# Kernel optimization log

Hardware: AMD Instinct MI355X
Metric: run time of the kernel (lower is better)

The kernel has to match this reference:

```python
import jax, jax.numpy as jnp
import numpy as np

B, S, T, H, E, V = 32, 400, 32, 512, 128, 50000
A = H  # attention feature dim

def setup_inputs() -> dict:
    key = jax.random.key(0)
    ks = jax.random.split(key, 16)
    f = lambda k, shape: jax.random.normal(k, shape, dtype=jnp.float32) * 0.02
    return {
        "source_tokens": jax.random.randint(ks[0], (B, S), 0, V, dtype=jnp.int32),
        "embedded_tgt": jax.random.normal(ks[1], (B, T, E), dtype=jnp.float32),
        "encoder_states": jax.random.normal(ks[2], (B, S, 2 * H), dtype=jnp.float32),
        "source_mask": jnp.ones((B, S), dtype=bool),
        "h0": f(ks[3], (B, H)),
        "c0": f(ks[4], (B, H)),
        "W_ih": f(ks[5], (4 * H, E)),
        "W_hh": f(ks[6], (4 * H, H)),
        "b_ih": jnp.zeros((4 * H,), jnp.float32),
        "b_hh": jnp.zeros((4 * H,), jnp.float32),
        "W_enc": f(ks[7], (2 * H, A)),
        "W_dec": f(ks[8], (H, A)),
        "w_cov": f(ks[9], (A,)),
        "b_att": jnp.zeros((A,), jnp.float32),
        "v_att": f(ks[10], (A,)),
        "W_ah": f(ks[11], (3 * H, H)),
        "b_ah": jnp.zeros((H,), jnp.float32),
        "W_pg": f(ks[12], (3 * H + E, 1)),
        "b_pg": jnp.zeros((1,), jnp.float32),
        "W_v": f(ks[13], (H, V)),
        "b_v": jnp.zeros((V,), jnp.float32),
    }


def reference(source_tokens, embedded_tgt, encoder_states, source_mask, h0, c0,
              W_ih, W_hh, b_ih, b_hh, W_enc, W_dec, w_cov, b_att, v_att,
              W_ah, b_ah, W_pg, b_pg, W_v, b_v):
    Bn, Sn = source_tokens.shape
    # precompute encoder projection for Bahdanau attention: (B,S,A)
    enc_proj = jnp.einsum('bsd,da->bsa', encoder_states, W_enc)
    bidx = jnp.arange(Bn)[:, None]
    NEG = jnp.float32(-1e9)
    EPS = jnp.float32(1e-20)

    def step(carry, emb):  # emb: (B,E)
        h, c, cov = carry
        # LSTM cell (torch gate order i,f,g,o)
        gates = emb @ W_ih.T + h @ W_hh.T + b_ih + b_hh
        i, fg, g, o = jnp.split(gates, 4, axis=-1)
        c = jax.nn.sigmoid(fg) * c + jax.nn.sigmoid(i) * jnp.tanh(g)
        h = jax.nn.sigmoid(o) * jnp.tanh(c)
        # coverage attention
        feat = jnp.tanh(enc_proj + (h @ W_dec)[:, None, :] + cov[:, :, None] * w_cov + b_att)
        scores = jnp.where(source_mask, feat @ v_att, NEG)  # (B,S)
        attn = jax.nn.softmax(scores, axis=-1)
        context = jnp.einsum('bs,bsd->bd', attn, encoder_states)  # (B,2H)
        cov = cov + attn
        ah = jnp.tanh(jnp.concatenate([context, h], axis=-1) @ W_ah + b_ah)  # (B,H)
        p_gen = jax.nn.sigmoid(jnp.concatenate([context, h, emb], axis=-1) @ W_pg + b_pg)  # (B,1)
        vocab_dist = p_gen * jax.nn.softmax(ah @ W_v + b_v, axis=-1)  # (B,V)
        attn_dist = (1.0 - p_gen) * attn  # (B,S)
        final = vocab_dist.at[bidx, source_tokens].add(attn_dist)  # copy-merge scatter_add
        logp = jnp.log(final + EPS)
        return (h, c, cov), (logp, ah, attn, cov, p_gen[:, 0])

    cov0 = jnp.zeros_like(source_mask, dtype=jnp.float32)
    _, (logps, dec_states, attns, covs, p_gens) = jax.lax.scan(
        step, (h0, c0, cov0), jnp.swapaxes(embedded_tgt, 0, 1))
    tr = lambda x: jnp.swapaxes(x, 0, 1)  # (T,B,...) -> (B,T,...)
    return tr(logps), tr(dec_states), tr(attns), tr(covs), tr(p_gens)
```

## Files before the change

kernel.cpp:

```cpp
#include <hip/hip_runtime.h>
#include <hip/hip_bf16.h>
#include <stdint.h>
#include <stddef.h>

#define B_  32
#define S_  400
#define T_  32
#define H_  512
#define E_  128
#define V_  50000
#define A_  512
#define H2_ 1024
#define H3_ 1536
#define H4_ 2048
#define R_  1024
#define PGK_ 1664
#define NBLKV_ 391
#define GRB_ 128
#define WROW_ 520

typedef unsigned short u16;
typedef short v8s __attribute__((ext_vector_type(8)));
typedef float v4f __attribute__((ext_vector_type(4)));

__device__ __forceinline__ float fsig(float x){ return 1.0f/(1.0f + __expf(-x)); }
__device__ __forceinline__ float ftanh(float x){ float e = __expf(2.0f*x); return 1.0f - 2.0f/(e + 1.0f); }
__device__ __forceinline__ u16 f2bf(float x){ __hip_bfloat16 b = __float2bfloat16(x); return *reinterpret_cast<u16*>(&b); }
__device__ __forceinline__ float bf2f(u16 u){ __hip_bfloat16 b = *reinterpret_cast<__hip_bfloat16*>(&u); return __bfloat162float(b); }

__device__ __forceinline__ float wsum(float v){
  #pragma unroll
  for (int off = 32; off > 0; off >>= 1) v += __shfl_xor(v, off, 64);
  return v;
}
__device__ __forceinline__ float wmax(float v){
  #pragma unroll
  for (int off = 32; off > 0; off >>= 1) v = fmaxf(v, __shfl_xor(v, off, 64));
  return v;
}

#define ALD(p)    __hip_atomic_load((p), __ATOMIC_RELAXED, __HIP_MEMORY_SCOPE_AGENT)
#define AST(p,v)  __hip_atomic_store((p), (v), __ATOMIC_RELAXED, __HIP_MEMORY_SCOPE_AGENT)

__device__ __forceinline__ void ldsbar(){
  asm volatile("s_waitcnt lgkmcnt(0)" ::: "memory");
  __builtin_amdgcn_s_barrier();
  asm volatile("" ::: "memory");
}

__device__ __forceinline__ void gridbar2(unsigned* bar, unsigned target, int grp){
  __syncthreads();
  if (threadIdx.x == 0){
    unsigned v = __hip_atomic_fetch_add(bar + grp*32, 1u, __ATOMIC_RELAXED, __HIP_MEMORY_SCOPE_AGENT);
    if (v == target*16u - 1u){
      unsigned g2 = __hip_atomic_fetch_add(bar + 256, 1u, __ATOMIC_RELAXED, __HIP_MEMORY_SCOPE_AGENT);
      if (g2 == target*8u - 1u)
        AST(bar + 288, target);
    }
    while (ALD(bar + 288) < target) __builtin_amdgcn_s_sleep(2);
    asm volatile("" ::: "memory");
  }
  __syncthreads();
}


__global__ void k_init0(unsigned* __restrict__ bar, unsigned long long* __restrict__ mz){
  int t = threadIdx.x;
  if (t < 512) AST(bar + t, 0u);
  if (t < 128) AST(mz + t, 0ull);
}

__global__ __launch_bounds__(256) void k_transpose(const float* __restrict__ in, float* __restrict__ out, int R, int C){
  __shared__ float tile[64][65];
  int c0 = blockIdx.x*64, r0 = blockIdx.y*64;
  int tid = threadIdx.x;
  int cl = tid & 63, q = tid >> 6;
  #pragma unroll
  for (int i=0;i<16;i++){
    int r = q + i*4;
    float v = 0.0f;
    if (r0 + r < R && c0 + cl < C) v = in[(size_t)(r0+r)*C + c0 + cl];
    tile[r][cl] = v;
  }
  __syncthreads();
  #pragma unroll
  for (int i=0;i<16;i++){
    int c = q + i*4;
    if (c0 + c < C && r0 + cl < R)
      out[(size_t)(c0+c)*R + r0 + cl] = tile[cl][c];
  }
}

__global__ __launch_bounds__(256) void k_convT(const float* __restrict__ in, u16* __restrict__ hi, int R, int C){
  __shared__ float tile[64][65];
  int c0 = blockIdx.x*64, r0 = blockIdx.y*64;
  int tid = threadIdx.x;
  int cl = tid & 63, q = tid >> 6;
  #pragma unroll
  for (int i=0;i<16;i++){
    int r = q + i*4;
    float v = 0.0f;
    if (r0 + r < R && c0 + cl < C) v = in[(size_t)(r0+r)*C + c0 + cl];
    tile[r][cl] = v;
  }
  __syncthreads();
  #pragma unroll
  for (int i=0;i<16;i++){
    int c = q + i*4;
    if (c0 + c < C && r0 + cl < R)
      hi[(size_t)(c0+c)*R + r0 + cl] = f2bf(tile[cl][c]);
  }
}

__global__ __launch_bounds__(256) void k_convT3(const float* __restrict__ in, u16* __restrict__ out){
  __shared__ float tile[64][65];
  int c0 = blockIdx.x*64, r0 = blockIdx.y*64;
  int tid = threadIdx.x;
  int cl = tid & 63, q = tid >> 6;
  #pragma unroll
  for (int i=0;i<16;i++){
    int r = q + i*4;
    tile[r][cl] = in[(size_t)(r0+r)*A_ + c0 + cl];
  }
  __syncthreads();
  #pragma unroll
  for (int i=0;i<16;i++){
    int c = q + i*4;
    float v = tile[cl][c];
    u16 h = f2bf(v);
    u16 lo = f2bf(v - bf2f(h));
    size_t o = (size_t)(c0+c)*3072 + (r0+cl);
    out[o] = h;
    out[o + 1024] = lo;
    out[o + 2048] = h;
  }
}

__global__ void k_conv3(const float* __restrict__ in, u16* __restrict__ out, int n4){
  int i = blockIdx.x*256 + threadIdx.x;
  if (i >= n4) return;
  float4 x = reinterpret_cast<const float4*>(in)[i];
  u16 h0v=f2bf(x.x), h1v=f2bf(x.y), h2v=f2bf(x.z), h3v=f2bf(x.w);
  uint2 hv; hv.x = (unsigned)h0v | ((unsigned)h1v << 16); hv.y = (unsigned)h2v | ((unsigned)h3v << 16);
  uint2 lv;
  lv.x = (unsigned)f2bf(x.x - bf2f(h0v)) | ((unsigned)f2bf(x.y - bf2f(h1v)) << 16);
  lv.y = (unsigned)f2bf(x.z - bf2f(h2v)) | ((unsigned)f2bf(x.w - bf2f(h3v)) << 16);
  int row = i >> 8, c = (i & 255)*4;
  size_t base = (size_t)row*3072 + c;
  *reinterpret_cast<uint2*>(out + base)        = hv;
  *reinterpret_cast<uint2*>(out + base + 1024) = hv;
  *reinterpret_cast<uint2*>(out + base + 2048) = lv;
}

__global__ __launch_bounds__(256) void k_gih(const float* __restrict__ emb, const float* __restrict__ WihT,
    const float* __restrict__ b_ih, const float* __restrict__ b_hh, float* __restrict__ G){
  __shared__ float em[8][128];
  int r0 = blockIdx.x*8;
  int tid = threadIdx.x;
  #pragma unroll
  for (int i=0;i<4;i++){
    int e = i*256 + tid;
    em[e>>7][e&127] = emb[(size_t)(r0 + (e>>7))*E_ + (e&127)];
  }
  __syncthreads();
  for (int jj=0;jj<8;jj++){
    int j = jj*256 + tid;
    float bias = b_ih[j] + b_hh[j];
    float acc[8];
    #pragma unroll
    for (int r=0;r<8;r++) acc[r] = bias;
    for (int e=0;e<128;e++){
      float wv = WihT[(size_t)e*H4_ + j];
      #pragma unroll
      for (int r=0;r<8;r++) acc[r] += em[r][e]*wv;
    }
    #pragma unroll
    for (int rr=0;rr<8;rr++){
      int r = r0 + rr;
      G[(size_t)(r & 31)*65536 + (size_t)(j >> 9)*16384 + (size_t)(j & 511)*32 + (r >> 5)] = acc[rr];
    }
  }
}

__global__ __launch_bounds__(256, 2) void k_gemm_bf16(
    const u16* __restrict__ A, int lda, const u16* __restrict__ Bt, int ldb,
    const float* __restrict__ bias, float* __restrict__ Cf, u16* __restrict__ Cbf, int ldc,
    int M, int N, int K, float2* __restrict__ stats, int nblk)
{
  __shared__ __align__(16) float CsF[128*132];
  __shared__ float rs[128], rs2[128];
  u16* As = reinterpret_cast<u16*>(CsF);
  u16* Bs = As + 128*64;
  const int tid = threadIdx.x;
  const int m0 = blockIdx.y * 128;
  const int n0 = blockIdx.x * 128;
  const int l  = tid & 63;
  const int wavebase = tid & ~63;
  const int wid = tid >> 6;
  const int wm = (wid >> 1) * 64;
  const int wn = (wid & 1) * 64;

  v4f acc[4][4];
  v4f vzero = {0.0f, 0.0f, 0.0f, 0.0f};
  #pragma unroll
  for (int i=0;i<4;i++)
    #pragma unroll
    for (int j=0;j<4;j++) acc[i][j] = vzero;

  for (int k0 = 0; k0 < K; k0 += 64){
    __syncthreads();
    #pragma unroll
    for (int jj=0;jj<4;jj++){
      int fc = jj*256 + tid;
      int row = fc >> 3;
      int cc = (fc & 7) ^ (row & 7);
      const u16* g = A + (size_t)(m0 + row)*lda + k0 + cc*8;
      __builtin_amdgcn_global_load_lds(
        (__attribute__((address_space(1))) void*)g,
        (__attribute__((address_space(3))) void*)(As + (size_t)(jj*256 + wavebase)*8),
        16, 0, 0);
    }
    #pragma unroll
    for (int jj=0;jj<4;jj++){
      int fc = jj*256 + tid;
      int row = fc >> 3;
      int cc = (fc & 7) ^ (row & 7);
      int rn = n0 + row; if (rn > N-1) rn = N-1;
      const u16* g = Bt + (size_t)rn*ldb + k0 + cc*8;
      __builtin_amdgcn_global_load_lds(
        (__attribute__((address_space(1))) void*)g,
        (__attribute__((address_space(3))) void*)(Bs + (size_t)(jj*256 + wavebase)*8),
        16, 0, 0);
    }
    __syncthreads();
    #pragma unroll
    for (int ks=0;ks<2;ks++){
      v8s af[4], bfr[4];
      #pragma unroll
      for (int rt=0;rt<4;rt++){
        int r = wm + rt*16 + (l & 15);
        int cs = (ks*4 + (l >> 4)) ^ (r & 7);
        af[rt] = *reinterpret_cast<const v8s*>(As + r*64 + cs*8);
      }
      #pragma unroll
      for (int nt=0;nt<4;nt++){
        int r = wn + nt*16 + (l & 15);
        int cs = (ks*4 + (l >> 4)) ^ (r & 7);
        bfr[nt] = *reinterpret_cast<const v8s*>(Bs + r*64 + cs*8);
      }
      #pragma unroll
      for (int rt=0;rt<4;rt++)
        #pragma unroll
        for (int nt=0;nt<4;nt++)
          acc[rt][nt] = __builtin_amdgcn_mfma_f32_16x16x32_bf16(af[rt], bfr[nt], acc[rt][nt], 0, 0, 0);
    }
  }

  const int cl = l & 15;
  const int rg = (l >> 4) * 4;
  float cvv[4][4][4];
  #pragma unroll
  for (int rt=0;rt<4;rt++)
    #pragma unroll
    for (int nt=0;nt<4;nt++){
      int gc = n0 + wn + nt*16 + cl;
      float bv = (bias && gc < N) ? bias[gc] : 0.0f;
      #pragma unroll
      for (int i=0;i<4;i++) cvv[rt][nt][i] = acc[rt][nt][i] + bv;
    }

  if (stats){
    float tsm[4][4];
    #pragma unroll
    for (int rt=0;rt<4;rt++)
      #pragma unroll
      for (int i=0;i<4;i++){
        float mx = -1e30f;
        #pragma unroll
        for (int nt=0;nt<4;nt++){
          int gc = n0 + wn + nt*16 + cl;
          if (gc < N) mx = fmaxf(mx, cvv[rt][nt][i]);
        }
        #pragma unroll
        for (int off=1; off<16; off<<=1) mx = fmaxf(mx, __shfl_xor(mx, off, 64));
        if (wn == 0 && cl == 0) rs[wm + rt*16 + rg + i] = mx;
        tsm[rt][i] = mx;
      }
    __syncthreads();
    if (wn != 0){
      #pragma unroll
      for (int rt=0;rt<4;rt++)
        #pragma unroll
        for (int i=0;i<4;i++){
          float c = fmaxf(tsm[rt][i], rs[wm + rt*16 + rg + i]);
          if (cl == 0) rs[wm + rt*16 + rg + i] = c;
        }
    }
    __syncthreads();
    #pragma unroll
    for (int rt=0;rt<4;rt++)
      #pragma unroll
      for (int i=0;i<4;i++){
        float rm = rs[wm + rt*16 + rg + i];
        float sm = 0.0f;
        #pragma unroll
        for (int nt=0;nt<4;nt++){
          int gc = n0 + wn + nt*16 + cl;
          if (gc < N) sm += __expf(cvv[rt][nt][i] - rm);
        }
        #pragma unroll
        for (int off=1; off<16; off<<=1) sm += __shfl_xor(sm, off, 64);
        tsm[rt][i] = sm;
        if (wn == 0 && cl == 0) rs2[wm + rt*16 + rg + i] = sm;
      }
    __syncthreads();
    if (wn != 0 && cl == 0){
      #pragma unroll
      for (int rt=0;rt<4;rt++)
        #pragma unroll
        for (int i=0;i<4;i++){
          int row = wm + rt*16 + rg + i;
          stats[(size_t)(m0 + row)*nblk + blockIdx.x] =
            make_float2(rs[row], tsm[rt][i] + rs2[row]);
        }
    }
  }

  __syncthreads();
  #pragma unroll
  for (int rt=0;rt<4;rt++)
    #pragma unroll
    for (int nt=0;nt<4;nt++)
      #pragma unroll
      for (int i=0;i<4;i++)
        CsF[(wm + rt*16 + rg + i)*132 + wn + nt*16 + cl] = cvv[rt][nt][i];
  __syncthreads();
  #pragma unroll
  for (int it=0; it<16; ++it){
    int row = (tid >> 5) + it*8;
    int c4 = tid & 31;
    int gc = n0 + c4*4;
    int gr = m0 + row;
    if (gc < N){
      float4 v = *reinterpret_cast<const float4*>(&CsF[row*132 + c4*4]);
      if (Cf) *reinterpret_cast<float4*>(Cf + (size_t)gr*ldc + gc) = v;
      if (Cbf){
        uint2 o;
        o.x = (unsigned)f2bf(v.x) | ((unsigned)f2bf(v.y) << 16);
        o.y = (unsigned)f2bf(v.z) | ((unsigned)f2bf(v.w) << 16);
        *reinterpret_cast<uint2*>(Cbf + (size_t)gr*ldc + gc) = o;
      }
    }
  }
}

__global__ __launch_bounds__(256) void k_wv_f32(
  const float* __restrict__ Aah, const float* __restrict__ Wv, const float* __restrict__ bv,
  float* __restrict__ Cl)
{
  __shared__ float Asf[32][68];
  __shared__ float Bsf[32][64];
  int n0 = blockIdx.x*64, m0 = blockIdx.y*64;
  int tid = threadIdx.x;
  int tx = tid & 15, ty = tid >> 4;
  float acc[4][4] = {};
  for (int kc = 0; kc < H_; kc += 32){
    __syncthreads();
    #pragma unroll
    for (int i=0;i<8;i++){
      int e = i*256 + tid;
      Asf[e & 31][e >> 5] = Aah[(size_t)(m0 + (e >> 5))*H_ + kc + (e & 31)];
    }
    #pragma unroll
    for (int i=0;i<8;i++){
      int e = i*256 + tid;
      int nc = n0 + (e & 63); if (nc >= V_) nc = V_-1;
      Bsf[e >> 6][e & 63] = Wv[(size_t)(kc + (e >> 6))*V_ + nc];
    }
    __syncthreads();
    #pragma unroll
    for (int k=0;k<32;k++){
      float4 a4 = *reinterpret_cast<const float4*>(&Asf[k][ty*4]);
      float4 b4 = *reinterpret_cast<const float4*>(&Bsf[k][tx*4]);
      float av[4] = {a4.x, a4.y, a4.z, a4.w};
      float bv4[4] = {b4.x, b4.y, b4.z, b4.w};
      #pragma unroll
      for (int i=0;i<4;i++)
        #pragma unroll
        for (int j=0;j<4;j++)
          acc[i][j] = __builtin_fmaf(av[i], bv4[j], acc[i][j]);
    }
  }
  #pragma unroll
  for (int i=0;i<4;i++){
    int rr = m0 + ty*4 + i;
    #pragma unroll
    for (int j=0;j<4;j++){
      int cc = n0 + tx*4 + j;
      if (cc < V_) Cl[(size_t)rr*V_ + cc] = acc[i][j] + bv[cc];
    }
  }
}

__global__ __launch_bounds__(1024) void k_recur(
  const float* __restrict__ W_hh, const float* __restrict__ G2,
  const float* __restrict__ W_decT, const u16* __restrict__ ep_bf,
  const float* __restrict__ w_cov, const float* __restrict__ v_att,
  const void* __restrict__ maskp, const float* __restrict__ h0,
  const float* __restrict__ c0, float* __restrict__ h_gT,
  float* __restrict__ dec_g, unsigned long long* __restrict__ mz,
  float* __restrict__ catbuf, float* __restrict__ attns, float* __restrict__ covs,
  unsigned* __restrict__ bar)
{
  const int beta = blockIdx.x;
  const int tid = threadIdx.x;
  __shared__ __align__(16) u16 Whi[32*WROW_];
  __shared__ __align__(16) u16 Wlo[32*WROW_];
  __shared__ __align__(16) u16 Hhi[32*WROW_];
  __shared__ __align__(16) u16 Hlo[32*WROW_];
  __shared__ float gv2[16][32];
  __shared__ float c_l[128];
  __shared__ float dec_l[512];
  __shared__ float sc_l[100];
  __shared__ float cov_l[100];
  __shared__ float smz[4][2];

  const int b32 = tid & 31;
  const int w = tid >> 6, l = tid & 63;
  const int grp = beta & 7;
  const int bb = (beta & 7)*4 + (beta >> 5);
  const int sq = (beta >> 3) & 3;
  const int b2 = (tid & 15)*2;
  const int kg = tid >> 4;

  for (int idx = tid; idx < 32*512; idx += 1024){
    int row = idx >> 9;
    int k = idx & 511;
    float v = 0.0f;
    if (row < 16)      v = W_hh[((size_t)(row >> 2)*H_ + beta*4 + (row & 3))*H_ + k];
    else if (row < 20) v = W_decT[(size_t)(beta*4 + (row - 16))*H_ + k];
    u16 h = f2bf(v);
    Whi[row*WROW_ + k] = h;
    Wlo[row*WROW_ + k] = f2bf(v - bf2f(h));
  }
  if (tid < 128) c_l[tid] = c0[(size_t)(tid & 31)*H_ + beta*4 + (tid >> 5)];
  if (tid < 100) cov_l[tid] = 0.f;

  const unsigned* m32p = (const unsigned*)maskp;
  const unsigned char* m8p = (const unsigned char*)maskp;
  const bool bytemode = (m32p[0] == 0x01010101u);

  float wc8[8], va8[8];
  {
    int a0 = l*8;
    #pragma unroll
    for (int j=0;j<8;j++){ wc8[j] = w_cov[a0+j]; va8[j] = v_att[a0+j]; }
  }

  float hA[8], hB[8];
  unsigned long long hld[8];
  #pragma unroll
  for (int kk=0;kk<8;kk++){
    int k = kg*8 + kk;
    hA[kk] = h0[(size_t)b2*H_ + k];
    hB[kk] = h0[(size_t)(b2+1)*H_ + k];
  }

  unsigned gen = 0;
  for (int i = 0; i <= T_; ++i){
    const int par = i & 1;
    {
      v8s phA, plA, phB, plB;
      #pragma unroll
      for (int kk=0;kk<8;kk++){
        float va = hA[kk], vb = hB[kk];
        u16 ha = f2bf(va), hb = f2bf(vb);
        phA[kk] = (short)ha; plA[kk] = (short)f2bf(va - bf2f(ha));
        phB[kk] = (short)hb; plB[kk] = (short)f2bf(vb - bf2f(hb));
      }
      *reinterpret_cast<v8s*>(Hhi + (size_t)b2*WROW_ + kg*8) = phA;
      *reinterpret_cast<v8s*>(Hlo + (size_t)b2*WROW_ + kg*8) = plA;
      *reinterpret_cast<v8s*>(Hhi + (size_t)(b2+1)*WROW_ + kg*8) = phB;
      *reinterpret_cast<v8s*>(Hlo + (size_t)(b2+1)*WROW_ + kg*8) = plB;
    }
    ldsbar();

    if (w < 4){
      const int mt = w >> 1, nt = w & 1;
      const int fr = (l & 15);
      const int fo = (l >> 4)*8;
      const u16* Ahi = Whi + (size_t)(mt*16 + fr)*WROW_ + fo;
      const u16* Alo = Wlo + (size_t)(mt*16 + fr)*WROW_ + fo;
      const u16* Bhi = Hhi + (size_t)(nt*16 + fr)*WROW_ + fo;
      const u16* Blo = Hlo + (size_t)(nt*16 + fr)*WROW_ + fo;
      v4f a0 = {0.f,0.f,0.f,0.f}, a1 = a0, a2 = a0;
      #pragma unroll
      for (int ks=0; ks<16; ks++){
        v8s wh = *reinterpret_cast<const v8s*>(Ahi + ks*32);
        v8s wl = *reinterpret_cast<const v8s*>(Alo + ks*32);
        v8s hh = *reinterpret_cast<const v8s*>(Bhi + ks*32);
        v8s hl = *reinterpret_cast<const v8s*>(Blo + ks*32);
        a0 = __builtin_amdgcn_mfma_f32_16x16x32_bf16(wh, hh, a0, 0, 0, 0);
        a1 = __builtin_amdgcn_mfma_f32_16x16x32_bf16(wh, hl, a1, 0, 0, 0);
        a2 = __builtin_amdgcn_mfma_f32_16x16x32_bf16(wl, hh, a2, 0, 0, 0);
      }
      v4f acc = a0 + a1 + a2;
      if (mt == 0){
        int col = nt*16 + fr;
        int r0w = (l >> 4)*4;
        #pragma unroll
        for (int q=0;q<4;q++) gv2[r0w + q][col] = acc[q];
      } else if ((l >> 4) == 0){
        int b = nt*16 + fr;
        float* dg = dec_g + (size_t)par*B_*A_ + (size_t)b*A_ + beta*4;
        unsigned long long p0 = ((unsigned long long)__float_as_uint(acc[1]) << 32) | __float_as_uint(acc[0]);
        unsigned long long p1 = ((unsigned long long)__float_as_uint(acc[3]) << 32) | __float_as_uint(acc[2]);
        AST(reinterpret_cast<unsigned long long*>(dg), p0);
        AST(reinterpret_cast<unsigned long long*>(dg + 2), p1);
      }
    }
    ldsbar();

    if (i < T_ && tid < 128){
      int hh = tid >> 5;
      int hidx = beta*4 + hh;
      const float* Gr = G2 + (size_t)i*65536 + (size_t)hidx*32 + b32;
      float gi = gv2[0*4+hh][b32] + Gr[0];
      float gf = gv2[1*4+hh][b32] + Gr[16384];
      float gz = gv2[2*4+hh][b32] + Gr[32768];
      float go = gv2[3*4+hh][b32] + Gr[49152];
      float co = c_l[tid];
      float cn = fsig(gf)*co + fsig(gi)*ftanh(gz);
      float hn = fsig(go)*ftanh(cn);
      c_l[tid] = cn;
      AST(h_gT + (size_t)(par^1)*16384 + (size_t)hidx*32 + b32, hn);
      catbuf[(size_t)(b32*T_ + i)*H3_ + H2_ + hidx] = hn;
    }
    gridbar2(bar, ++gen, grp);

    if (i < T_){
      const unsigned long long* hp =
        reinterpret_cast<const unsigned long long*>(h_gT + (size_t)(par^1)*16384);
      #pragma unroll
      for (int kk=0;kk<8;kk++)
        hld[kk] = ALD(hp + (size_t)(kg*8 + kk)*16 + (b2 >> 1));
    }

    if (i > 0){
      const int r = bb*T_ + (i-1);
      if (tid < 512) dec_l[tid] = ALD(dec_g + (size_t)par*B_*A_ + (size_t)bb*A_ + tid);
      ldsbar();
      int a0i = l*8;
      float dec8[8];
      #pragma unroll
      for (int j=0;j<8;j++) dec8[j] = dec_l[a0i+j];
      #pragma unroll
      for (int it=0; it<7; ++it){
        int sl = w + it*16;
        if (sl < 100){
          int s = sq*100 + sl;
          float cv = cov_l[sl];
          uint4 e8 = *reinterpret_cast<const uint4*>(ep_bf + (size_t)(bb*S_ + s)*A_ + a0i);
          unsigned uu[4] = {e8.x, e8.y, e8.z, e8.w};
          float part = 0.f;
          #pragma unroll
          for (int j=0;j<4;j++){
            float xa = bf2f((u16)(uu[j] & 0xFFFFu)) + dec8[2*j]   + cv*wc8[2*j];
            part += va8[2*j]*ftanh(xa);
            float xb = bf2f((u16)(uu[j] >> 16))     + dec8[2*j+1] + cv*wc8[2*j+1];
            part += va8[2*j+1]*ftanh(xb);
          }
          part = wsum(part);
          if (l == 0){
            bool on = bytemode ? (m8p[bb*S_+s] != 0) : (m32p[bb*S_+s] != 0u);
            sc_l[sl] = on ? part : -1e9f;
          }
        }
      }
      __syncthreads();
      if (tid < 64){
        float x1v = sc_l[l];
        float x2v = (l + 64 < 100) ? sc_l[l + 64] : -1e30f;
        float m = wmax(fmaxf(x1v, x2v));
        float z = __expf(x1v - m) + ((l + 64 < 100) ? __expf(x2v - m) : 0.f);
        z = wsum(z);
        if (l == 0){
          unsigned zt = (__float_as_uint(z) & ~255u) | (gen & 255u);
          unsigned long long pk = ((unsigned long long)zt << 32) | (unsigned long long)__float_as_uint(m);
          AST(mz + bb*4 + sq, pk);
        }
      }
      if (tid < 4){
        unsigned long long v;
        do {
          v = ALD(mz + bb*4 + tid);
          if (((unsigned)(v >> 32) & 255u) == (gen & 255u)) break;
          __builtin_amdgcn_s_sleep(1);
        } while (true);
        smz[tid][0] = __uint_as_float((unsigned)v);
        smz[tid][1] = __uint_as_float((unsigned)(v >> 32));
      }
      __syncthreads();
      float gm = fmaxf(fmaxf(smz[0][0], smz[1][0]), fmaxf(smz[2][0], smz[3][0]));
      float gZ = smz[0][1]*__expf(smz[0][0]-gm) + smz[1][1]*__expf(smz[1][0]-gm)
               + smz[2][1]*__expf(smz[2][0]-gm) + smz[3][1]*__expf(smz[3][0]-gm);
      float invZ = 1.f/gZ;
      if (tid < 100){
        float av = __expf(sc_l[tid] - gm)*invZ;
        int s = sq*100 + tid;
        float cn = cov_l[tid] + av;
        cov_l[tid] = cn;
        attns[(size_t)r*S_ + s] = av;
        covs[(size_t)r*S_ + s]  = cn;
      }
      __syncthreads();
    }

    if (i < T_){
      #pragma unroll
      for (int kk=0;kk<8;kk++){
        hA[kk] = __uint_as_float((unsigned)hld[kk]);
        hB[kk] = __uint_as_float((unsigned)(hld[kk] >> 32));
      }
    }
  }
}


__global__ __launch_bounds__(256, 2) void k_ctx(
  const float* __restrict__ attns, const float* __restrict__ enc, float* __restrict__ catbuf)
{
  __shared__ float att_s[32][400];
  int d0 = blockIdx.x*64, b = blockIdx.y;
  int tid = threadIdx.x;
  for (int tt=0; tt<32; ++tt)
    for (int s = tid; s < S_; s += 256)
      att_s[tt][s] = attns[(size_t)(b*T_ + tt)*S_ + s];
  __syncthreads();
  int d = d0 + (tid & 63);
  int t0 = (tid >> 6)*8;
  float acc[8] = {0,0,0,0,0,0,0,0};
  const float* encb = enc + (size_t)b*S_*H2_ + d;
  #pragma unroll 4
  for (int s=0; s<S_; ++s){
    float ev = encb[(size_t)s*H2_];
    #pragma unroll
    for (int i=0;i<8;i++) acc[i] = __builtin_fmaf(att_s[t0+i][s], ev, acc[i]);
  }
  #pragma unroll
  for (int i=0;i<8;i++)
    catbuf[(size_t)(b*T_ + t0 + i)*H3_ + d] = acc[i];
}

__global__ __launch_bounds__(256) void k_ahgemm(
  const float* __restrict__ Acat, const float* __restrict__ W_ah, const float* __restrict__ b_ah,
  float* __restrict__ dec_states, u16* __restrict__ ah_bf)
{
  __shared__ float Asf[32][68];
  __shared__ float Bsf[32][64];
  int n0 = blockIdx.x*64, m0 = blockIdx.y*64;
  int tid = threadIdx.x;
  int tx = tid & 15, ty = tid >> 4;
  float acc[4][4] = {};
  for (int kc = 0; kc < H3_; kc += 32){
    __syncthreads();
    #pragma unroll
    for (int i=0;i<8;i++){
      int e = i*256 + tid;
      Asf[e & 31][e >> 5] = Acat[(size_t)(m0 + (e >> 5))*H3_ + kc + (e & 31)];
    }
    #pragma unroll
    for (int i=0;i<8;i++){
      int e = i*256 + tid;
      Bsf[e >> 6][e & 63] = W_ah[(size_t)(kc + (e >> 6))*H_ + n0 + (e & 63)];
    }
    __syncthreads();
    #pragma unroll
    for (int k=0;k<32;k++){
      float4 a4 = *reinterpret_cast<const float4*>(&Asf[k][ty*4]);
      float4 b4 = *reinterpret_cast<const float4*>(&Bsf[k][tx*4]);
      float av[4] = {a4.x, a4.y, a4.z, a4.w};
      float bv[4] = {b4.x, b4.y, b4.z, b4.w};
      #pragma unroll
      for (int i=0;i<4;i++)
        #pragma unroll
        for (int j=0;j<4;j++)
          acc[i][j] = __builtin_fmaf(av[i], bv[j], acc[i][j]);
    }
  }
  #pragma unroll
  for (int i=0;i<4;i++){
    int rr = m0 + ty*4 + i;
    #pragma unroll
    for (int j=0;j<4;j++){
      int cc = n0 + tx*4 + j;
      float v = ftanh(acc[i][j] + b_ah[cc]);
      dec_states[(size_t)rr*H_ + cc] = v;
      if (ah_bf) ah_bf[(size_t)rr*H_ + cc] = f2bf(v);
    }
  }
}

__global__ __launch_bounds__(512) void k_pgen(const float* __restrict__ catbuf, const float* __restrict__ emb,
  const float* __restrict__ W_pg, const float* __restrict__ b_pg, float* __restrict__ pgens)
{
  int w = threadIdx.x >> 6, l = threadIdx.x & 63;
  int r = blockIdx.x*8 + w;
  float part = 0.0f;
  for (int d = l; d < PGK_; d += 64){
    float x = (d < H3_) ? catbuf[(size_t)r*H3_ + d] : emb[(size_t)r*E_ + (d - H3_)];
    part += x*W_pg[d];
  }
  part = wsum(part);
  if (l == 0) pgens[r] = fsig(part + b_pg[0]);
}

__global__ __launch_bounds__(512) void k_final2(
  float* __restrict__ logits, const float* __restrict__ pgens,
  const float* __restrict__ attns, const int* __restrict__ src,
  const float2* __restrict__ stats, int nblk)
{
  __shared__ unsigned bits[1568];
  __shared__ unsigned keys[1024];
  __shared__ float vals[1024];
  __shared__ float sred[18];
  int r = blockIdx.x;
  int b = r >> 5;
  int tid = threadIdx.x;
  int w = tid >> 6, l = tid & 63;
  float* row = logits + (size_t)r*V_;

  for (int i = tid; i < 1568; i += 512) bits[i] = 0u;
  for (int i = tid; i < 1024; i += 512){ keys[i] = 0xFFFFFFFFu; vals[i] = 0.0f; }

  if (stats){
    float m = -1e30f, Z = 0.0f;
    if (tid < nblk){ float2 st = stats[(size_t)r*nblk + tid]; m = st.x; Z = st.y; }
    #pragma unroll
    for (int off=32; off>0; off>>=1){
      float mo = __shfl_xor(m, off, 64);
      float Zo = __shfl_xor(Z, off, 64);
      float nm = fmaxf(m, mo);
      Z = Z*__expf(m - nm) + Zo*__expf(mo - nm);
      m = nm;
    }
    if (l == 0){ sred[w*2] = m; sred[w*2+1] = Z; }
    __syncthreads();
    if (tid == 0){
      float gm = -1e30f, gz = 0.0f;
      #pragma unroll
      for (int i=0;i<8;i++){
        float mi = sred[i*2], zi = sred[i*2+1];
        float nm = fmaxf(gm, mi);
        gz = gz*__expf(gm - nm) + zi*__expf(mi - nm);
        gm = nm;
      }
      sred[16] = gm; sred[17] = gz;
    }
    __syncthreads();
  } else {
    float m = -1e30f;
    for (int j = tid; j < V_/4; j += 512){
      float4 x = reinterpret_cast<const float4*>(row)[j];
      m = fmaxf(fmaxf(m, x.x), fmaxf(fmaxf(x.y, x.z), x.w));
    }
    m = wmax(m);
    if (l == 0) sred[w] = m;
    __syncthreads();
    if (tid == 0){
      float gm = -1e30f;
      #pragma unroll
      for (int i=0;i<8;i++) gm = fmaxf(gm, sred[i]);
      sred[16] = gm;
    }
    __syncthreads();
    float gm = sred[16];
    float z = 0.0f;
    for (int j = tid; j < V_/4; j += 512){
      float4 x = reinterpret_cast<const float4*>(row)[j];
      z += __expf(x.x-gm) + __expf(x.y-gm) + __expf(x.z-gm) + __expf(x.w-gm);
    }
    z = wsum(z);
    if (l == 0) sred[8 + w] = z;
    __syncthreads();
    if (tid == 0){
      float gz = 0.0f;
      #pragma unroll
      for (int i=0;i<8;i++) gz += sred[8 + i];
      sred[17] = gz;
    }
    __syncthreads();
  }

  float gm = sred[16];
  float gZ = sred[17];
  float pg = pgens[r];
  float scale = pg / gZ;
  float lscale = __logf(scale);

  if (tid < S_){
    int tok = src[b*S_ + tid];
    float add = (1.0f - pg)*attns[(size_t)r*S_ + tid];
    atomicOr(&bits[tok >> 5], 1u << (tok & 31));
    unsigned h = ((unsigned)tok * 2654435761u) >> 22;
    while (true){
      unsigned prev = atomicCAS(&keys[h], 0xFFFFFFFFu, (unsigned)tok);
      if (prev == 0xFFFFFFFFu || prev == (unsigned)tok){
        atomicAdd(&vals[h], add);
        break;
      }
      h = (h + 1) & 1023;
    }
  }
  __syncthreads();

  for (int j = tid; j < V_/4; j += 512){
    float4 x = reinterpret_cast<const float4*>(row)[j];
    int v = 4*j;
    float o[4];
    float xv[4] = {x.x, x.y, x.z, x.w};
    #pragma unroll
    for (int k=0;k<4;k++){
      int vv = v + k;
      bool hit = (bits[vv >> 5] >> (vv & 31)) & 1u;
      float tt = xv[k] - gm + lscale;
      if (!hit && tt > -25.0f){
        o[k] = tt;
      } else {
        float pval = __expf(xv[k] - gm)*scale;
        if (hit){
          unsigned h = ((unsigned)vv * 2654435761u) >> 22;
          while (keys[h] != 0xFFFFFFFFu){
            if (keys[h] == (unsigned)vv){ pval += vals[h]; break; }
            h = (h + 1) & 1023;
          }
        }
        o[k] = __logf(pval + 1e-20f);
      }
    }
    reinterpret_cast<float4*>(row)[j] = make_float4(o[0], o[1], o[2], o[3]);
  }
}


extern "C" void kernel_launch(void* const* d_in, const int* in_sizes, int n_in,
                              void* d_out, int out_size, void* d_ws, size_t ws_size,
                              hipStream_t stream)
{
  const int* src_tokens = (const int*)d_in[0];
  const float* embedded = (const float*)d_in[1];
  const float* enc      = (const float*)d_in[2];
  const void*  maskp    = (const void*)d_in[3];
  const float* h0  = (const float*)d_in[4];
  const float* c0  = (const float*)d_in[5];
  const float* W_ih = (const float*)d_in[6];
  const float* W_hh = (const float*)d_in[7];
  const float* b_ih = (const float*)d_in[8];
  const float* b_hh = (const float*)d_in[9];
  const float* W_enc = (const float*)d_in[10];
  const float* W_dec = (const float*)d_in[11];
  const float* w_cov = (const float*)d_in[12];
  const float* b_att = (const float*)d_in[13];
  const float* v_att = (const float*)d_in[14];
  const float* W_ah  = (const float*)d_in[15];
  const float* b_ah  = (const float*)d_in[16];
  const float* W_pg  = (const float*)d_in[17];
  const float* b_pg  = (const float*)d_in[18];
  const float* W_v   = (const float*)d_in[19];
  const float* b_v   = (const float*)d_in[20];
  (void)in_sizes; (void)n_in; (void)out_size;

  float* outp = (float*)d_out;
  float* logps = outp;
  float* dec_states = logps + (size_t)R_*V_;
  float* attns = dec_states + (size_t)R_*H_;
  float* covs  = attns + (size_t)R_*S_;
  float* pgens = covs + (size_t)R_*S_;

  char* sp = (char*)logps;
  auto salloc = [&](size_t bytes) -> void* {
    void* p = (void*)sp;
    sp += (bytes + 255) & ~(size_t)255;
    return p;
  };
  unsigned* bar = (unsigned*)salloc(2048);
  unsigned long long* mz = (unsigned long long*)salloc((size_t)B_*4*8);
  u16* ep_bf    = (u16*)salloc((size_t)B_*S_*A_*2);
  u16* enc3     = (u16*)salloc((size_t)B_*S_*3072*2);
  u16* WencT3   = (u16*)salloc((size_t)A_*3072*2);
  float* WihT   = (float*)salloc((size_t)E_*H4_*4);
  float* W_decT = (float*)salloc((size_t)H_*A_*4);
  float* G2     = (float*)salloc((size_t)R_*H4_*4);
  float* catbuf = (float*)salloc((size_t)R_*H3_*4);
  float* dec_g  = (float*)salloc((size_t)2*B_*A_*4);
  float* h_gT   = (float*)salloc((size_t)2*H_*B_*4);

  char* wp = (char*)d_ws;
  auto walloc = [&](size_t bytes) -> void* {
    void* p = (void*)wp;
    wp += (bytes + 255) & ~(size_t)255;
    return p;
  };
  u16* ah_bf = (u16*)walloc((size_t)R_*H_*2);
  u16* WvT   = (u16*)walloc((size_t)V_*H_*2);
  float2* stats = (float2*)walloc((size_t)R_*NBLKV_*8);
  const size_t ws_fast  = (size_t)R_*H_*2 + (size_t)V_*H_*2 + 512;
  const size_t ws_stats = ws_fast + (size_t)R_*NBLKV_*8 + 256;
  const bool fast_wv   = (ws_size >= ws_fast);
  const bool use_stats = (ws_size >= ws_stats);

  k_init0<<<1, 512, 0, stream>>>(bar, mz);
  k_transpose<<<dim3(2,32), 256, 0, stream>>>(W_ih, WihT, H4_, E_);
  k_transpose<<<dim3(8,8), 256, 0, stream>>>(W_dec, W_decT, H_, A_);
  k_gih<<<128, 256, 0, stream>>>(embedded, WihT, b_ih, b_hh, G2);
  k_conv3<<<(B_*S_*H2_/4 + 255)/256, 256, 0, stream>>>(enc, enc3, B_*S_*H2_/4);
  k_convT3<<<dim3(8,16), 256, 0, stream>>>(W_enc, WencT3);
  if (fast_wv)
    k_convT<<<dim3((V_+63)/64, 8), 256, 0, stream>>>(W_v, WvT, H_, V_);

  k_gemm_bf16<<<dim3(A_/128, (B_*S_)/128), 256, 0, stream>>>(
      enc3, 3072, WencT3, 3072, b_att, nullptr, ep_bf, A_, B_*S_, A_, 3072, nullptr, 0);

  k_recur<<<GRB_, 1024, 0, stream>>>(W_hh, G2, W_decT, ep_bf, w_cov, v_att, maskp,
                                     h0, c0, h_gT, dec_g, mz,
                                     catbuf, attns, covs, bar);

  k_ctx<<<dim3(16, 32), 256, 0, stream>>>(attns, enc, catbuf);
  k_ahgemm<<<dim3(8,16), 256, 0, stream>>>(catbuf, W_ah, b_ah, dec_states, fast_wv ? ah_bf : (u16*)nullptr);
  k_pgen<<<128, 512, 0, stream>>>(catbuf, embedded, W_pg, b_pg, pgens);

  if (fast_wv)
    k_gemm_bf16<<<dim3(NBLKV_, R_/128), 256, 0, stream>>>(
        ah_bf, H_, WvT, H_, b_v, logps, nullptr, V_, R_, V_, H_,
        use_stats ? stats : nullptr, NBLKV_);
  else
    k_wv_f32<<<dim3((V_+63)/64, R_/64), 256, 0, stream>>>(dec_states, W_v, b_v, logps);

  k_final2<<<R_, 512, 0, stream>>>(logps, pgens, attns, src_tokens,
                                   (fast_wv && use_stats) ? stats : nullptr, NBLKV_);
}
```

Baseline: 1.194 ms.

## Split recurrent kernel into LSTM producer blocks and per-batch attention consumer blocks

The persistent recurrence kernel is split into 128 LSTM blocks and 32 attention blocks, one per batch row. The LSTM blocks advance through timesteps writing per-step h and decoder projections to step-indexed buffers, and only the LSTM blocks arrive at the barrier. Attention blocks poll the barrier one step behind and compute the full 400-position softmax locally, which removes the cross-block max/sum exchange. This takes attention off the LSTM critical path and lets the two run pipelined, at the cost of more grid blocks, per-step history buffers, and each attention block doing 4x more positions serially.

```diff
diff --git a/kernel.cpp b/kernel.cpp
--- a/kernel.cpp
+++ b/kernel.cpp
@@ -16,7 +16,8 @@
 #define R_  1024
 #define PGK_ 1664
 #define NBLKV_ 391
-#define GRB_ 128
+#define GRBX_ 128
+#define GRB_  160
 #define WROW_ 520
 
 typedef unsigned short u16;
@@ -48,8 +49,7 @@
   asm volatile("" ::: "memory");
 }
 
-__device__ __forceinline__ void gridbar2(unsigned* bar, unsigned target, int grp){
-  __syncthreads();
+__device__ __forceinline__ void arrive(unsigned* bar, unsigned target, int grp){
   if (threadIdx.x == 0){
     unsigned v = __hip_atomic_fetch_add(bar + grp*32, 1u, __ATOMIC_RELAXED, __HIP_MEMORY_SCOPE_AGENT);
     if (v == target*16u - 1u){
@@ -57,6 +57,10 @@
       if (g2 == target*8u - 1u)
         AST(bar + 288, target);
     }
+  }
+}
+__device__ __forceinline__ void pollgate(unsigned* bar, unsigned target){
+  if (threadIdx.x == 0){
     while (ALD(bar + 288) < target) __builtin_amdgcn_s_sleep(2);
     asm volatile("" ::: "memory");
   }
@@ -64,10 +68,9 @@
 }
 
 
-__global__ void k_init0(unsigned* __restrict__ bar, unsigned long long* __restrict__ mz){
+__global__ void k_init0(unsigned* __restrict__ bar){
   int t = threadIdx.x;
   if (t < 512) AST(bar + t, 0u);
-  if (t < 128) AST(mz + t, 0ull);
 }
 
 __global__ __launch_bounds__(256) void k_transpose(const float* __restrict__ in, float* __restrict__ out, int R, int C){
@@ -407,8 +410,8 @@
   const float* __restrict__ W_decT, const u16* __restrict__ ep_bf,
   const float* __restrict__ w_cov, const float* __restrict__ v_att,
   const void* __restrict__ maskp, const float* __restrict__ h0,
-  const float* __restrict__ c0, float* __restrict__ h_gT,
-  float* __restrict__ dec_g, unsigned long long* __restrict__ mz,
+  const float* __restrict__ c0, float* __restrict__ h_steps,
+  float* __restrict__ dec_steps,
   float* __restrict__ catbuf, float* __restrict__ attns, float* __restrict__ covs,
   unsigned* __restrict__ bar)
 {
@@ -421,207 +424,202 @@
   __shared__ float gv2[16][32];
   __shared__ float c_l[128];
   __shared__ float dec_l[512];
-  __shared__ float sc_l[100];
-  __shared__ float cov_l[100];
-  __shared__ float smz[4][2];
+  __shared__ float sc_l[400];
+  __shared__ float cov_l[400];
+  __shared__ float red[16];
 
   const int b32 = tid & 31;
   const int w = tid >> 6, l = tid & 63;
-  const int grp = beta & 7;
-  const int bb = (beta & 7)*4 + (beta >> 5);
-  const int sq = (beta >> 3) & 3;
-  const int b2 = (tid & 15)*2;
-  const int kg = tid >> 4;
-
-  for (int idx = tid; idx < 32*512; idx += 1024){
-    int row = idx >> 9;
-    int k = idx & 511;
-    float v = 0.0f;
-    if (row < 16)      v = W_hh[((size_t)(row >> 2)*H_ + beta*4 + (row & 3))*H_ + k];
-    else if (row < 20) v = W_decT[(size_t)(beta*4 + (row - 16))*H_ + k];
-    u16 h = f2bf(v);
-    Whi[row*WROW_ + k] = h;
-    Wlo[row*WROW_ + k] = f2bf(v - bf2f(h));
-  }
-  if (tid < 128) c_l[tid] = c0[(size_t)(tid & 31)*H_ + beta*4 + (tid >> 5)];
-  if (tid < 100) cov_l[tid] = 0.f;
-
-  const unsigned* m32p = (const unsigned*)maskp;
-  const unsigned char* m8p = (const unsigned char*)maskp;
-  const bool bytemode = (m32p[0] == 0x01010101u);
-
-  float wc8[8], va8[8];
-  {
-    int a0 = l*8;
-    #pragma unroll
-    for (int j=0;j<8;j++){ wc8[j] = w_cov[a0+j]; va8[j] = v_att[a0+j]; }
-  }
-
-  float hA[8], hB[8];
-  unsigned long long hld[8];
-  #pragma unroll
-  for (int kk=0;kk<8;kk++){
-    int k = kg*8 + kk;
-    hA[kk] = h0[(size_t)b2*H_ + k];
-    hB[kk] = h0[(size_t)(b2+1)*H_ + k];
-  }
-
-  unsigned gen = 0;
-  for (int i = 0; i <= T_; ++i){
-    const int par = i & 1;
+
+  if (beta < GRBX_){
+    const int grp = beta & 7;
+    const int b2 = (tid & 15)*2;
+    const int kg = tid >> 4;
+
+    for (int idx = tid; idx < 32*512; idx += 1024){
+      int row = idx >> 9;
+      int k = idx & 511;
+      float v = 0.0f;
+      if (row < 16)      v = W_hh[((size_t)(row >> 2)*H_ + beta*4 + (row & 3))*H_ + k];
+      else if (row < 20) v = W_decT[(size_t)(beta*4 + (row - 16))*H_ + k];
+      u16 h = f2bf(v);
+      Whi[row*WROW_ + k] = h;
+      Wlo[row*WROW_ + k] = f2bf(v - bf2f(h));
+    }
+    if (tid < 128) c_l[tid] = c0[(size_t)(tid & 31)*H_ + beta*4 + (tid >> 5)];
+
+    float hA[8], hB[8];
+    #pragma unroll
+    for (int kk=0;kk<8;kk++){
+      int k = kg*8 + kk;
+      hA[kk] = h0[(size_t)b2*H_ + k];
+      hB[kk] = h0[(size_t)(b2+1)*H_ + k];
+    }
+    __syncthreads();
+
+    for (int i = 0; i <= T_; ++i){
+      if (i > 0){
+        pollgate(bar, (unsigned)i);
+        unsigned long long hld[8];
+        const unsigned long long* hp =
+          reinterpret_cast<const unsigned long long*>(h_steps + (size_t)i*16384);
+        #pragma unroll
+        for (int kk=0;kk<8;kk++)
+          hld[kk] = ALD(hp + (size_t)(kg*8 + kk)*16 + (b2 >> 1));
+        #pragma unroll
+        for (int kk=0;kk<8;kk++){
+          hA[kk] = __uint_as_float((unsigned)hld[kk]);
+          hB[kk] = __uint_as_float((unsigned)(hld[kk] >> 32));
+        }
+      }
+      {
+        v8s phA, plA, phB, plB;
+        #pragma unroll
+        for (int kk=0;kk<8;kk++){
+          float va = hA[kk], vb = hB[kk];
+          u16 ha = f2bf(va), hb = f2bf(vb);
+          phA[kk] = (short)ha; plA[kk] = (short)f2bf(va - bf2f(ha));
+          phB[kk] = (short)hb; plB[kk] = (short)f2bf(vb - bf2f(hb));
+        }
+        *reinterpret_cast<v8s*>(Hhi + (size_t)b2*WROW_ + kg*8) = phA;
+        *reinterpret_cast<v8s*>(Hlo + (size_t)b2*WROW_ + kg*8) = plA;
+        *reinterpret_cast<v8s*>(Hhi + (size_t)(b2+1)*WROW_ + kg*8) = phB;
+        *reinterpret_cast<v8s*>(Hlo + (size_t)(b2+1)*WROW_ + kg*8) = plB;
+      }
+      ldsbar();
+
+      if (w < 4){
+        const int mt = w >> 1, nt = w & 1;
+        const int fr = (l & 15);
+        const int fo = (l >> 4)*8;
+        const u16* Ahi = Whi + (size_t)(mt*16 + fr)*WROW_ + fo;
+        const u16* Alo = Wlo + (size_t)(mt*16 + fr)*WROW_ + fo;
+        const u16* Bhi = Hhi + (size_t)(nt*16 + fr)*WROW_ + fo;
+        const u16* Blo = Hlo + (size_t)(nt*16 + fr)*WROW_ + fo;
+        v4f a0 = {0.f,0.f,0.f,0.f}, a1 = a0, a2 = a0;
+        #pragma unroll
+        for (int ks=0; ks<16; ks++){
+          v8s wh = *reinterpret_cast<const v8s*>(Ahi + ks*32);
+          v8s wl = *reinterpret_cast<const v8s*>(Alo + ks*32);
+          v8s hh = *reinterpret_cast<const v8s*>(Bhi + ks*32);
+          v8s hl = *reinterpret_cast<const v8s*>(Blo + ks*32);
+          a0 = __builtin_amdgcn_mfma_f32_16x16x32_bf16(wh, hh, a0, 0, 0, 0);
+          a1 = __builtin_amdgcn_mfma_f32_16x16x32_bf16(wh, hl, a1, 0, 0, 0);
+          a2 = __builtin_amdgcn_mfma_f32_16x16x32_bf16(wl, hh, a2, 0, 0, 0);
+        }
+        v4f acc = a0 + a1 + a2;
+        if (mt == 0){
+          int col = nt*16 + fr;
+          int r0w = (l >> 4)*4;
+          #pragma unroll
+          for (int q=0;q<4;q++) gv2[r0w + q][col] = acc[q];
+        } else if ((l >> 4) == 0 && i > 0){
+          int b = nt*16 + fr;
+          float* dg = dec_steps + (size_t)(i-1)*B_*A_ + (size_t)b*A_ + beta*4;
+          unsigned long long p0 = ((unsigned long long)__float_as_uint(acc[1]) << 32) | __float_as_uint(acc[0]);
+          unsigned long long p1 = ((unsigned long long)__float_as_uint(acc[3]) << 32) | __float_as_uint(acc[2]);
+          AST(reinterpret_cast<unsigned long long*>(dg), p0);
+          AST(reinterpret_cast<unsigned long long*>(dg + 2), p1);
+        }
+      }
+      ldsbar();
+
+      if (i < T_ && tid < 128){
+        int hh = tid >> 5;
+        int hidx = beta*4 + hh;
+        const float* Gr = G2 + (size_t)i*65536 + (size_t)hidx*32 + b32;
+        float gi = gv2[0*4+hh][b32] + Gr[0];
+        float gf = gv2[1*4+hh][b32] + Gr[16384];
+        float gz = gv2[2*4+hh][b32] + Gr[32768];
+        float go = gv2[3*4+hh][b32] + Gr[49152];
+        float co = c_l[tid];
+        float cn = fsig(gf)*co + fsig(gi)*ftanh(gz);
+        float hn = fsig(go)*ftanh(cn);
+        c_l[tid] = cn;
+        AST(h_steps + (size_t)(i+1)*16384 + (size_t)hidx*32 + b32, hn);
+        catbuf[(size_t)(b32*T_ + i)*H3_ + H2_ + hidx] = hn;
+      }
+      __syncthreads();
+      arrive(bar, (unsigned)(i+1), grp);
+    }
+  } else {
+    const int bb = beta - GRBX_;
+    if (tid < 400) cov_l[tid] = 0.f;
+
+    const unsigned* m32p = (const unsigned*)maskp;
+    const unsigned char* m8p = (const unsigned char*)maskp;
+    const bool bytemode = (m32p[0] == 0x01010101u);
+
+    float wc8[8], va8[8];
     {
-      v8s phA, plA, phB, plB;
-      #pragma unroll
-      for (int kk=0;kk<8;kk++){
-        float va = hA[kk], vb = hB[kk];
-        u16 ha = f2bf(va), hb = f2bf(vb);
-        phA[kk] = (short)ha; plA[kk] = (short)f2bf(va - bf2f(ha));
-        phB[kk] = (short)hb; plB[kk] = (short)f2bf(vb - bf2f(hb));
-      }
-      *reinterpret_cast<v8s*>(Hhi + (size_t)b2*WROW_ + kg*8) = phA;
-      *reinterpret_cast<v8s*>(Hlo + (size_t)b2*WROW_ + kg*8) = plA;
-      *reinterpret_cast<v8s*>(Hhi + (size_t)(b2+1)*WROW_ + kg*8) = phB;
-      *reinterpret_cast<v8s*>(Hlo + (size_t)(b2+1)*WROW_ + kg*8) = plB;
-    }
-    ldsbar();
-
-    if (w < 4){
-      const int mt = w >> 1, nt = w & 1;
-      const int fr = (l & 15);
-      const int fo = (l >> 4)*8;
-      const u16* Ahi = Whi + (size_t)(mt*16 + fr)*WROW_ + fo;
-      const u16* Alo = Wlo + (size_t)(mt*16 + fr)*WROW_ + fo;
-      const u16* Bhi = Hhi + (size_t)(nt*16 + fr)*WROW_ + fo;
-      const u16* Blo = Hlo + (size_t)(nt*16 + fr)*WROW_ + fo;
-      v4f a0 = {0.f,0.f,0.f,0.f}, a1 = a0, a2 = a0;
-      #pragma unroll
-      for (int ks=0; ks<16; ks++){
-        v8s wh = *reinterpret_cast<const v8s*>(Ahi + ks*32);
-        v8s wl = *reinterpret_cast<const v8s*>(Alo + ks*32);
-        v8s hh = *reinterpret_cast<const v8s*>(Bhi + ks*32);
-        v8s hl = *reinterpret_cast<const v8s*>(Blo + ks*32);
-        a0 = __builtin_amdgcn_mfma_f32_16x16x32_bf16(wh, hh, a0, 0, 0, 0);
-        a1 = __builtin_amdgcn_mfma_f32_16x16x32_bf16(wh, hl, a1, 0, 0, 0);
-        a2 = __builtin_amdgcn_mfma_f32_16x16x32_bf16(wl, hh, a2, 0, 0, 0);
-      }
-      v4f acc = a0 + a1 + a2;
-      if (mt == 0){
-        int col = nt*16 + fr;
-        int r0w = (l >> 4)*4;
-        #pragma unroll
-        for (int q=0;q<4;q++) gv2[r0w + q][col] = acc[q];
-      } else if ((l >> 4) == 0){
-        int b = nt*16 + fr;
-        float* dg = dec_g + (size_t)par*B_*A_ + (size_t)b*A_ + beta*4;
-        unsigned long long p0 = ((unsigned long long)__float_as_uint(acc[1]) << 32) | __float_as_uint(acc[0]);
-        unsigned long long p1 = ((unsigned long long)__float_as_uint(acc[3]) << 32) | __float_as_uint(acc[2]);
-        AST(reinterpret_cast<unsigned long long*>(dg), p0);
-        AST(reinterpret_cast<unsigned long long*>(dg + 2), p1);
-      }
-    }
-    ldsbar();
-
-    if (i < T_ && tid < 128){
-      int hh = tid >> 5;
-      int hidx = beta*4 + hh;
-      const float* Gr = G2 + (size_t)i*65536 + (size_t)hidx*32 + b32;
-      float gi = gv2[0*4+hh][b32] + Gr[0];
-      float gf = gv2[1*4+hh][b32] + Gr[16384];
-      float gz = gv2[2*4+hh][b32] + Gr[32768];
-      float go = gv2[3*4+hh][b32] + Gr[49152];
-      float co = c_l[tid];
-      float cn = fsig(gf)*co + fsig(gi)*ftanh(gz);
-      float hn = fsig(go)*ftanh(cn);
-      c_l[tid] = cn;
-      AST(h_gT + (size_t)(par^1)*16384 + (size_t)hidx*32 + b32, hn);
-      catbuf[(size_t)(b32*T_ + i)*H3_ + H2_ + hidx] = hn;
-    }
-    gridbar2(bar, ++gen, grp);
-
-    if (i < T_){
-      const unsigned long long* hp =
-        reinterpret_cast<const unsigned long long*>(h_gT + (size_t)(par^1)*16384);
-      #pragma unroll
-      for (int kk=0;kk<8;kk++)
-        hld[kk] = ALD(hp + (size_t)(kg*8 + kk)*16 + (b2 >> 1));
-    }
-
-    if (i > 0){
-      const int r = bb*T_ + (i-1);
-      if (tid < 512) dec_l[tid] = ALD(dec_g + (size_t)par*B_*A_ + (size_t)bb*A_ + tid);
+      int a0 = l*8;
+      #pragma unroll
+      for (int j=0;j<8;j++){ wc8[j] = w_cov[a0+j]; va8[j] = v_att[a0+j]; }
+    }
+    __syncthreads();
+
+    for (int s = 0; s < T_; ++s){
+      pollgate(bar, (unsigned)(s + 2));
+      if (tid < 256){
+        unsigned long long v = ALD(reinterpret_cast<const unsigned long long*>(
+            dec_steps + (size_t)s*B_*A_ + (size_t)bb*A_) + tid);
+        dec_l[tid*2]   = __uint_as_float((unsigned)v);
+        dec_l[tid*2+1] = __uint_as_float((unsigned)(v >> 32));
+      }
       ldsbar();
       int a0i = l*8;
       float dec8[8];
       #pragma unroll
       for (int j=0;j<8;j++) dec8[j] = dec_l[a0i+j];
-      #pragma unroll
-      for (int it=0; it<7; ++it){
+      #pragma unroll 5
+      for (int it=0; it<25; ++it){
         int sl = w + it*16;
-        if (sl < 100){
-          int s = sq*100 + sl;
-          float cv = cov_l[sl];
-          uint4 e8 = *reinterpret_cast<const uint4*>(ep_bf + (size_t)(bb*S_ + s)*A_ + a0i);
-          unsigned uu[4] = {e8.x, e8.y, e8.z, e8.w};
-          float part = 0.f;
-          #pragma unroll
-          for (int j=0;j<4;j++){
-            float xa = bf2f((u16)(uu[j] & 0xFFFFu)) + dec8[2*j]   + cv*wc8[2*j];
-            part += va8[2*j]*ftanh(xa);
-            float xb = bf2f((u16)(uu[j] >> 16))     + dec8[2*j+1] + cv*wc8[2*j+1];
-            part += va8[2*j+1]*ftanh(xb);
-          }
-          part = wsum(part);
-          if (l == 0){
-            bool on = bytemode ? (m8p[bb*S_+s] != 0) : (m32p[bb*S_+s] != 0u);
-            sc_l[sl] = on ? part : -1e9f;
-          }
+        float cv = cov_l[sl];
+        uint4 e8 = *reinterpret_cast<const uint4*>(ep_bf + (size_t)(bb*S_ + sl)*A_ + a0i);
+        unsigned uu[4] = {e8.x, e8.y, e8.z, e8.w};
+        float part = 0.f;
+        #pragma unroll
+        for (int j=0;j<4;j++){
+          float xa = bf2f((u16)(uu[j] & 0xFFFFu)) + dec8[2*j]   + cv*wc8[2*j];
+          part += va8[2*j]*ftanh(xa);
+          float xb = bf2f((u16)(uu[j] >> 16))     + dec8[2*j+1] + cv*wc8[2*j+1];
+          part += va8[2*j+1]*ftanh(xb);
+        }
+        part = wsum(part);
+        if (l == 0){
+          bool on = bytemode ? (m8p[bb*S_+sl] != 0) : (m32p[bb*S_+sl] != 0u);
+          sc_l[sl] = on ? part : -1e9f;
         }
       }
       __syncthreads();
-      if (tid < 64){
-        float x1v = sc_l[l];
-        float x2v = (l + 64 < 100) ? sc_l[l + 64] : -1e30f;
-        float m = wmax(fmaxf(x1v, x2v));
-        float z = __expf(x1v - m) + ((l + 64 < 100) ? __expf(x2v - m) : 0.f);
-        z = wsum(z);
-        if (l == 0){
-          unsigned zt = (__float_as_uint(z) & ~255u) | (gen & 255u);
-          unsigned long long pk = ((unsigned long long)zt << 32) | (unsigned long long)__float_as_uint(m);
-          AST(mz + bb*4 + sq, pk);
-        }
-      }
-      if (tid < 4){
-        unsigned long long v;
-        do {
-          v = ALD(mz + bb*4 + tid);
-          if (((unsigned)(v >> 32) & 255u) == (gen & 255u)) break;
-          __builtin_amdgcn_s_sleep(1);
-        } while (true);
-        smz[tid][0] = __uint_as_float((unsigned)v);
-        smz[tid][1] = __uint_as_float((unsigned)(v >> 32));
+      float x = (tid < 400) ? sc_l[tid] : -1e30f;
+      if (w < 7){
+        float m = wmax(x);
+        if (l == 0) red[w] = m;
       }
       __syncthreads();
-      float gm = fmaxf(fmaxf(smz[0][0], smz[1][0]), fmaxf(smz[2][0], smz[3][0]));
-      float gZ = smz[0][1]*__expf(smz[0][0]-gm) + smz[1][1]*__expf(smz[1][0]-gm)
-               + smz[2][1]*__expf(smz[2][0]-gm) + smz[3][1]*__expf(smz[3][0]-gm);
+      float gm = red[0];
+      #pragma unroll
+      for (int j=1;j<7;j++) gm = fmaxf(gm, red[j]);
+      float z = (tid < 400) ? __expf(x - gm) : 0.f;
+      if (w < 7){
+        float zs = wsum(z);
+        if (l == 0) red[8 + w] = zs;
+      }
+      __syncthreads();
+      float gZ = red[8];
+      #pragma unroll
+      for (int j=9;j<15;j++) gZ += red[j];
       float invZ = 1.f/gZ;
-      if (tid < 100){
-        float av = __expf(sc_l[tid] - gm)*invZ;
-        int s = sq*100 + tid;
+      int r = bb*T_ + s;
+      if (tid < 400){
+        float av = z*invZ;
         float cn = cov_l[tid] + av;
         cov_l[tid] = cn;
-        attns[(size_t)r*S_ + s] = av;
-        covs[(size_t)r*S_ + s]  = cn;
+        attns[(size_t)r*S_ + tid] = av;
+        covs[(size_t)r*S_ + tid]  = cn;
       }
       __syncthreads();
-    }
-
-    if (i < T_){
-      #pragma unroll
-      for (int kk=0;kk<8;kk++){
-        hA[kk] = __uint_as_float((unsigned)hld[kk]);
-        hB[kk] = __uint_as_float((unsigned)(hld[kk] >> 32));
-      }
     }
   }
 }
@@ -884,7 +882,6 @@
     return p;
   };
   unsigned* bar = (unsigned*)salloc(2048);
-  unsigned long long* mz = (unsigned long long*)salloc((size_t)B_*4*8);
   u16* ep_bf    = (u16*)salloc((size_t)B_*S_*A_*2);
   u16* enc3     = (u16*)salloc((size_t)B_*S_*3072*2);
   u16* WencT3   = (u16*)salloc((size_t)A_*3072*2);
@@ -892,8 +889,8 @@
   float* W_decT = (float*)salloc((size_t)H_*A_*4);
   float* G2     = (float*)salloc((size_t)R_*H4_*4);
   float* catbuf = (float*)salloc((size_t)R_*H3_*4);
-  float* dec_g  = (float*)salloc((size_t)2*B_*A_*4);
-  float* h_gT   = (float*)salloc((size_t)2*H_*B_*4);
+  float* h_steps   = (float*)salloc((size_t)(T_+1)*H_*B_*4);
+  float* dec_steps = (float*)salloc((size_t)T_*B_*A_*4);
 
   char* wp = (char*)d_ws;
   auto walloc = [&](size_t bytes) -> void* {
@@ -909,7 +906,7 @@
   const bool fast_wv   = (ws_size >= ws_fast);
   const bool use_stats = (ws_size >= ws_stats);
 
-  k_init0<<<1, 512, 0, stream>>>(bar, mz);
+  k_init0<<<1, 512, 0, stream>>>(bar);
   k_transpose<<<dim3(2,32), 256, 0, stream>>>(W_ih, WihT, H4_, E_);
   k_transpose<<<dim3(8,8), 256, 0, stream>>>(W_dec, W_decT, H_, A_);
   k_gih<<<128, 256, 0, stream>>>(embedded, WihT, b_ih, b_hh, G2);
@@ -922,7 +919,7 @@
       enc3, 3072, WencT3, 3072, b_att, nullptr, ep_bf, A_, B_*S_, A_, 3072, nullptr, 0);
 
   k_recur<<<GRB_, 1024, 0, stream>>>(W_hh, G2, W_decT, ep_bf, w_cov, v_att, maskp,
-                                     h0, c0, h_gT, dec_g, mz,
+                                     h0, c0, h_steps, dec_steps,
                                      catbuf, attns, covs, bar);
 
   k_ctx<<<dim3(16, 32), 256, 0, stream>>>(attns, enc, catbuf);
```

Measured after the change: 1.783 ms. 1.49x slower.
